# Kernel tuning notes

Measured on AMD Instinct MI355X. Metric: run time of the kernel, lower is better.

Reference implementation:

```python
import jax, jax.numpy as jnp
import numpy as np

DIM = 768   # embedding dim
NH = 12     # num heads
HD = DIM // NH  # head dim = 64
WS = 14     # window size
EPS = 1e-5  # nn.LayerNorm default


def _ln(x, w, b):
    m = jnp.mean(x, -1, keepdims=True)
    v = jnp.var(x, -1, keepdims=True)
    return (x - m) * jax.lax.rsqrt(v + EPS) * w + b


def setup_inputs() -> dict:
    key = jax.random.key(0)
    ks = jax.random.split(key, 8)
    def n(k, shape, s=0.02):
        return jax.random.normal(k, shape, jnp.float32) * s
    return {
        "x": jax.random.normal(ks[0], (4, 64, 64, DIM), jnp.float32),
        "ln1_w": jnp.ones((DIM,), jnp.float32),
        "ln1_b": jnp.zeros((DIM,), jnp.float32),
        "qkv_w": n(ks[1], (DIM, 3 * DIM)),
        "qkv_b": jnp.zeros((3 * DIM,), jnp.float32),
        "proj_w": n(ks[2], (DIM, DIM)),
        "proj_b": jnp.zeros((DIM,), jnp.float32),
        "rel_pos_h": n(ks[3], (2 * WS - 1, HD)),
        "rel_pos_w": n(ks[4], (2 * WS - 1, HD)),
        "ln2_w": jnp.ones((DIM,), jnp.float32),
        "ln2_b": jnp.zeros((DIM,), jnp.float32),
        "fc1_w": n(ks[5], (DIM, 4 * DIM)),
        "fc1_b": jnp.zeros((4 * DIM,), jnp.float32),
        "fc2_w": n(ks[6], (4 * DIM, DIM)),
        "fc2_b": jnp.zeros((DIM,), jnp.float32),
    }


def _block(x, ln1_w, ln1_b, qkv_w, qkv_b, proj_w, proj_b,
           rel_pos_h, rel_pos_w, ln2_w, ln2_b, fc1_w, fc1_b, fc2_w, fc2_b):
    B, H, W, C = x.shape
    shortcut = x
    xn = _ln(x, ln1_w, ln1_b)

    # ---- window partition (pad H,W up to multiples of WS) ----
    pad_h = (-H) % WS
    pad_w = (-W) % WS
    xp = jnp.pad(xn, ((0, 0), (0, pad_h), (0, pad_w), (0, 0)))
    Hp, Wp = H + pad_h, W + pad_w
    nh, nw = Hp // WS, Wp // WS
    xw = xp.reshape(B, nh, WS, nw, WS, C).transpose(0, 1, 3, 2, 4, 5)
    xw = xw.reshape(B * nh * nw, WS, WS, C)  # [Bw, ws, ws, C]
    Bw = B * nh * nw
    N = WS * WS

    # ---- attention with decomposed relative position bias ----
    qkv = xw.reshape(Bw, N, C) @ qkv_w + qkv_b            # [Bw, N, 3C]
    qkv = qkv.reshape(Bw, N, 3, NH, HD).transpose(2, 0, 3, 1, 4)  # [3, Bw, NH, N, HD]
    q, k, v = qkv[0], qkv[1], qkv[2]
    scale = HD ** -0.5
    attn = jnp.einsum("bhnd,bhmd->bhnm", q * scale, k)    # [Bw, NH, N, N]

    # decomposed rel pos: Rh[q_h, k_h, c], Rw[q_w, k_w, c]
    idx = jnp.arange(WS)[:, None] - jnp.arange(WS)[None, :] + (WS - 1)
    Rh = rel_pos_h[idx]  # [ws, ws, HD]
    Rw = rel_pos_w[idx]  # [ws, ws, HD]
    rq = q.reshape(Bw, NH, WS, WS, HD)
    rel_h = jnp.einsum("bnhwc,hkc->bnhwk", rq, Rh)  # over q rows vs k rows
    rel_w = jnp.einsum("bnhwc,wkc->bnhwk", rq, Rw)  # over q cols vs k cols
    attn = (attn.reshape(Bw, NH, WS, WS, WS, WS)
            + rel_h[..., :, None] + rel_w[..., None, :]).reshape(Bw, NH, N, N)

    attn = jax.nn.softmax(attn, axis=-1)
    out = jnp.einsum("bhnm,bhmd->bhnd", attn, v)          # [Bw, NH, N, HD]
    out = out.transpose(0, 2, 1, 3).reshape(Bw, WS, WS, C)
    out = out @ proj_w + proj_b

    # ---- window unpartition + crop padding ----
    out = out.reshape(B, nh, nw, WS, WS, C).transpose(0, 1, 3, 2, 4, 5)
    out = out.reshape(B, Hp, Wp, C)[:, :H, :W, :]

    x = shortcut + out

    # ---- MLP ----
    h = _ln(x, ln2_w, ln2_b)
    h = jax.nn.gelu(h @ fc1_w + fc1_b, approximate=False)
    x = x + (h @ fc2_w + fc2_b)
    return x


def reference(x, ln1_w, ln1_b, qkv_w, qkv_b, proj_w, proj_b,
              rel_pos_h, rel_pos_w, ln2_w, ln2_b, fc1_w, fc1_b, fc2_w, fc2_b):
    return _block(x, ln1_w, ln1_b, qkv_w, qkv_b, proj_w, proj_b,
                  rel_pos_h, rel_pos_w, ln2_w, ln2_b, fc1_w, fc1_b, fc2_w, fc2_b)
```

## Files before the change

kernel.cpp:

```cpp
#include <hip/hip_runtime.h>

typedef unsigned short u16;
typedef __bf16 bf16x8_t __attribute__((ext_vector_type(8)));
typedef float f32x4_t __attribute__((ext_vector_type(4)));

__device__ __forceinline__ float bf2f(u16 u) {
    union { unsigned u; float f; } c; c.u = ((unsigned)u) << 16; return c.f;
}
__device__ __forceinline__ u16 f2bf(float f) {
    union { float f; unsigned u; } c; c.f = f;
    unsigned u = c.u;
    unsigned r = (u + 0x7FFFu + ((u >> 16) & 1u)) >> 16;
    return (u16)r;
}

__device__ __forceinline__ void gld16(const u16* g, u16* l) {
    __builtin_amdgcn_global_load_lds(
        (const __attribute__((address_space(1))) unsigned*)g,
        (__attribute__((address_space(3))) unsigned*)l, 16, 0, 0);
}

__global__ __launch_bounds__(256) void ln1_window(
    const float* __restrict__ x, const float* __restrict__ w, const float* __restrict__ b,
    u16* __restrict__ out, int row0)
{
    int wv = threadIdx.x >> 6, lane = threadIdx.x & 63;
    int lrow = blockIdx.x * 4 + wv;
    int wr = row0 + lrow;
    int wb = wr / 196, t = wr % 196;
    int gh = ((wb % 25) / 5) * 14 + t / 14;
    int gw = (wb % 5) * 14 + t % 14;
    size_t orow = (size_t)lrow * 768;
    if (gh >= 64 || gw >= 64) {
        uint2 zz; zz.x = 0u; zz.y = 0u;
        for (int seg = 0; seg < 3; seg++)
            *(uint2*)&out[orow + seg * 256 + lane * 4] = zz;
        return;
    }
    size_t base = (size_t)(((wb / 25) * 64 + gh) * 64 + gw) * 768;
    f32x4_t v[3];
    float s = 0.f, sq = 0.f;
    for (int seg = 0; seg < 3; seg++) {
        v[seg] = *(const f32x4_t*)&x[base + seg * 256 + lane * 4];
        for (int j = 0; j < 4; j++) { s += v[seg][j]; sq += v[seg][j] * v[seg][j]; }
    }
    for (int o = 32; o > 0; o >>= 1) { s += __shfl_xor(s, o); sq += __shfl_xor(sq, o); }
    float mean = s * (1.0f / 768.0f);
    float var  = sq * (1.0f / 768.0f) - mean * mean;
    float inv  = rsqrtf(var + 1e-5f);
    for (int seg = 0; seg < 3; seg++) {
        f32x4_t w4 = *(const f32x4_t*)&w[seg * 256 + lane * 4];
        f32x4_t b4 = *(const f32x4_t*)&b[seg * 256 + lane * 4];
        u16 o0 = f2bf((v[seg][0] - mean) * inv * w4[0] + b4[0]);
        u16 o1 = f2bf((v[seg][1] - mean) * inv * w4[1] + b4[1]);
        u16 o2 = f2bf((v[seg][2] - mean) * inv * w4[2] + b4[2]);
        u16 o3 = f2bf((v[seg][3] - mean) * inv * w4[3] + b4[3]);
        uint2 pv; pv.x = (unsigned)o0 | ((unsigned)o1 << 16);
        pv.y = (unsigned)o2 | ((unsigned)o3 << 16);
        *(uint2*)&out[orow + seg * 256 + lane * 4] = pv;
    }
}

__global__ __launch_bounds__(256) void ln2_chunk(
    const float* __restrict__ xin, const float* __restrict__ w, const float* __restrict__ b,
    u16* __restrict__ out)
{
    int wv = threadIdx.x >> 6, lane = threadIdx.x & 63;
    int row = blockIdx.x * 4 + wv;
    size_t base = (size_t)row * 768;
    f32x4_t v[3];
    float s = 0.f, sq = 0.f;
    for (int seg = 0; seg < 3; seg++) {
        v[seg] = *(const f32x4_t*)&xin[base + seg * 256 + lane * 4];
        for (int j = 0; j < 4; j++) { s += v[seg][j]; sq += v[seg][j] * v[seg][j]; }
    }
    for (int o = 32; o > 0; o >>= 1) { s += __shfl_xor(s, o); sq += __shfl_xor(sq, o); }
    float mean = s * (1.0f / 768.0f);
    float var  = sq * (1.0f / 768.0f) - mean * mean;
    float inv  = rsqrtf(var + 1e-5f);
    for (int seg = 0; seg < 3; seg++) {
        f32x4_t w4 = *(const f32x4_t*)&w[seg * 256 + lane * 4];
        f32x4_t b4 = *(const f32x4_t*)&b[seg * 256 + lane * 4];
        u16 o0 = f2bf((v[seg][0] - mean) * inv * w4[0] + b4[0]);
        u16 o1 = f2bf((v[seg][1] - mean) * inv * w4[1] + b4[1]);
        u16 o2 = f2bf((v[seg][2] - mean) * inv * w4[2] + b4[2]);
        u16 o3 = f2bf((v[seg][3] - mean) * inv * w4[3] + b4[3]);
        uint2 pv; pv.x = (unsigned)o0 | ((unsigned)o1 << 16);
        pv.y = (unsigned)o2 | ((unsigned)o3 << 16);
        *(uint2*)&out[base + seg * 256 + lane * 4] = pv;
    }
}

__global__ __launch_bounds__(256) void transpose_wf(
    const float* __restrict__ in, u16* __restrict__ out, int K, int N)
{
    __shared__ u16 t[32][33];
    __shared__ u16 tt[32][32];
    int n0 = blockIdx.x * 32, k0 = blockIdx.y * 32;
    int tx = threadIdx.x & 31, ty = threadIdx.x >> 5;
    for (int q = 0; q < 4; q++) {
        int k = k0 + ty + q * 8, n = n0 + tx;
        t[ty + q * 8][tx] = (k < K && n < N) ? f2bf(in[(size_t)k * N + n]) : (u16)0;
    }
    __syncthreads();
    for (int q = 0; q < 4; q++) tt[ty + q * 8][tx] = t[tx][ty + q * 8];
    __syncthreads();
    if (threadIdx.x < 128) {
        int r = threadIdx.x >> 2, c8 = (threadIdx.x & 3) << 3;
        int n = n0 + r, k = k0 + c8;
        if (n < N && k < K)
            *(uint4*)&out[(size_t)n * K + k] = *(const uint4*)&tt[r][c8];
    }
}

__global__ __launch_bounds__(256) void build_relT(
    const float* __restrict__ rh, const float* __restrict__ rw, u16* __restrict__ out)
{
    int i = blockIdx.x * 256 + threadIdx.x;
    int r = i >> 6, c = i & 63;
    float v = (r < 27) ? rh[r * 64 + c] : (r < 54 ? rw[(r - 27) * 64 + c] : 0.f);
    out[i] = f2bf(v);
}

__global__ __launch_bounds__(256) void build_vt(
    const u16* __restrict__ qkvc, u16* __restrict__ vt)
{
    int z = blockIdx.x;
    int wb = z / 12, h = z % 12;
    __shared__ u16 t[64][232];
    int tid = threadIdx.x;
    for (int base = 0; base < 196; base += 4) {
        int m = base + (tid >> 6);
        int d = tid & 63;
        t[d][m] = qkvc[(size_t)(wb * 196 + m) * 2304 + 1536 + h * 64 + d];
    }
    for (int idx = tid; idx < 28 * 64; idx += 256) {
        int m = 196 + idx / 64, d = idx % 64;
        t[d][m] = 0;
    }
    __syncthreads();
    size_t ob = (size_t)z * 64 * 224;
    for (int idx = tid; idx < 64 * 28; idx += 256) {
        int d = idx / 28, c8 = (idx % 28) << 3;
        *(uint4*)&vt[ob + (size_t)d * 224 + c8] = *(const uint4*)&t[d][c8];
    }
}

__global__ __launch_bounds__(256) void softmax_rel2(
    u16* __restrict__ S, const u16* __restrict__ G2)
{
    int z = blockIdx.y;
    int wv = threadIdx.x >> 6, lane = threadIdx.x & 63;
    int nbase = blockIdx.x * 28 + wv * 7;
    for (int i = 0; i < 7; i++) {
        int n = nbase + i;
        size_t srow = (size_t)z * 196 * 224 + (size_t)n * 224;
        const u16* g2 = G2 + (size_t)z * 196 * 64 + (size_t)n * 64;
        int qh = n / 14, qw = n % 14;
        float s[4];
        for (int c = 0; c < 4; c++) {
            int m = c * 64 + lane;
            if (m < 196) {
                int kk = m / 14, jj = m % 14;
                float bh = bf2f(g2[qh - kk + 13]);
                float bw = bf2f(g2[27 + qw - jj + 13]);
                s[c] = 0.125f * bf2f(S[srow + m]) + bh + bw;
            } else s[c] = -1e30f;
        }
        float mx = fmaxf(fmaxf(s[0], s[1]), fmaxf(s[2], s[3]));
        for (int o = 32; o > 0; o >>= 1) mx = fmaxf(mx, __shfl_xor(mx, o));
        float e[4], sm = 0.f;
        for (int c = 0; c < 4; c++) {
            int m = c * 64 + lane;
            e[c] = (m < 196) ? expf(s[c] - mx) : 0.f;
            sm += e[c];
        }
        for (int o = 32; o > 0; o >>= 1) sm += __shfl_xor(sm, o);
        float inv = 1.0f / sm;
        for (int c = 0; c < 4; c++) {
            int m = c * 64 + lane;
            if (m < 224) S[srow + m] = f2bf(e[c] * inv);
        }
    }
}

__device__ __forceinline__ int swz_off(int row, int kcElem) {
    return row * 32 + (kcElem ^ (((row >> 1) & 3) << 3));
}

template <int MODE>
__global__ __launch_bounds__(256, (MODE == 1 || MODE == 2 || MODE == 6) ? 3 : 4)
void gemm_nt(
    const u16* __restrict__ Aall, const u16* __restrict__ Ball,
    const float* __restrict__ bias, const float* xf,
    u16* __restrict__ Cb, float* Cf, int M, int row0)
{
    constexpr int BK = 32;
    constexpr bool DEEP = (MODE == 1 || MODE == 2 || MODE == 6);
    int N, K, lda, ldb;
    size_t aoff = 0, boff = 0, coff = 0;
    if constexpr (MODE == 0) { N = 2304; K = 768; lda = 768; ldb = 768; }
    else if constexpr (MODE == 1) {
        N = 196; K = 64; lda = 2304; ldb = 2304;
        int z = blockIdx.z;
        aoff = (size_t)(z / 12) * 196 * 2304 + (size_t)(z % 12) * 64;
        boff = aoff + 768;
        coff = (size_t)z * 196 * 224;
    } else if constexpr (MODE == 2) {
        N = 64; K = 224; lda = 224; ldb = 224;
        int z = blockIdx.z;
        aoff = (size_t)z * 196 * 224;
        boff = (size_t)z * 64 * 224;
        coff = (size_t)(z / 12) * 196 * 768 + (size_t)(z % 12) * 64;
    } else if constexpr (MODE == 3) { N = 768; K = 768; lda = 768; ldb = 768; }
    else if constexpr (MODE == 4) { N = 3072; K = 768; lda = 768; ldb = 768; }
    else if constexpr (MODE == 6) {
        N = 64; K = 64; lda = 2304; ldb = 64;
        int z = blockIdx.z;
        aoff = (size_t)(z / 12) * 196 * 2304 + (size_t)(z % 12) * 64;
        boff = 0;
        coff = (size_t)z * 196 * 64;
    }
    else { N = 768; K = 3072; lda = 3072; ldb = 3072; }

    constexpr int NBUF = DEEP ? 3 : 2;
    __shared__ __align__(16) u16 smem[NBUF * 8192];

    int tid = threadIdx.x, wid = tid >> 6, lane = tid & 63;
    int quad = lane >> 4, l16 = lane & 15;

    int bx = blockIdx.x, by = blockIdx.y;
    if constexpr (MODE != 1 && MODE != 2 && MODE != 6) {
        int gX = gridDim.x;
        int nwg = gX * gridDim.y;
        int orig = by * gX + bx;
        int q = nwg >> 3, r = nwg & 7;
        int xcd = orig & 7, idx = orig >> 3;
        int wg = (xcd < r ? xcd * (q + 1) : r * (q + 1) + (xcd - r) * q) + idx;
        bx = wg % gX; by = wg / gX;
    }
    int m_tile = by * 128, n_tile = bx * 128;
    int wm0 = (wid >> 1) * 64, wn0 = (wid & 1) * 64;

    const u16* A = Aall + aoff;
    const u16* B = Ball + boff;

    const u16* gA[2]; const u16* gB[2];
    int loff[2];
    {
        int s = lane & 3, rofs = lane >> 2;
        for (int j = 0; j < 2; j++) {
            int r0 = wid * 32 + j * 16;
            int rr = r0 + rofs;
            int xr = (rr >> 1) & 3;
            int colo = ((s ^ xr) << 3);
            int am = m_tile + rr; if (am > M - 1) am = M - 1;
            int bn = n_tile + rr; if (bn > N - 1) bn = N - 1;
            gA[j] = A + (size_t)am * lda + colo;
            gB[j] = B + (size_t)bn * ldb + colo;
            loff[j] = r0 * 32;
        }
    }

    f32x4_t acc[4][4];
    f32x4_t z4 = {0.f, 0.f, 0.f, 0.f};
    for (int mt = 0; mt < 4; mt++)
        for (int nt = 0; nt < 4; nt++) acc[mt][nt] = z4;

    if constexpr (!DEEP) {
        for (int j = 0; j < 2; j++) {
            gld16(gA[j], smem + loff[j]);
            gld16(gB[j], smem + 4096 + loff[j]);
        }
        int cur = 0;
        for (int k0 = 0; k0 < K; k0 += BK) {
            __syncthreads();
            int boffc = cur << 13;
            if (k0 + BK < K) {
                int boffn = boffc ^ 8192;
                for (int j = 0; j < 2; j++) {
                    gld16(gA[j] + k0 + BK, smem + boffn + loff[j]);
                    gld16(gB[j] + k0 + BK, smem + boffn + 4096 + loff[j]);
                }
            }
            const u16* Ac = smem + boffc;
            const u16* Bc = smem + boffc + 4096;
            bf16x8_t af[4], bfv[4];
            for (int t = 0; t < 4; t++) {
                int ar = wm0 + t * 16 + l16;
                int br = wn0 + t * 16 + l16;
                af[t]  = *(const bf16x8_t*)&Ac[swz_off(ar, quad * 8)];
                bfv[t] = *(const bf16x8_t*)&Bc[swz_off(br, quad * 8)];
            }
            for (int mt = 0; mt < 4; mt++)
                for (int nt = 0; nt < 4; nt++)
                    acc[mt][nt] = __builtin_amdgcn_mfma_f32_16x16x32_bf16(
                        af[mt], bfv[nt], acc[mt][nt], 0, 0, 0);
            cur ^= 1;
        }
    } else {
        int nsteps = K / BK;
        for (int j = 0; j < 2; j++) {
            gld16(gA[j], smem + loff[j]);
            gld16(gB[j], smem + 4096 + loff[j]);
        }
        for (int j = 0; j < 2; j++) {
            gld16(gA[j] + BK, smem + 8192 + loff[j]);
            gld16(gB[j] + BK, smem + 12288 + loff[j]);
        }
        int cur = 0;
        for (int k = 0; k < nsteps; k++) {
            if (k + 1 < nsteps) {
                asm volatile("s_waitcnt vmcnt(4)" ::: "memory");
            } else {
                asm volatile("s_waitcnt vmcnt(0)" ::: "memory");
            }
            __builtin_amdgcn_sched_barrier(0);
            __builtin_amdgcn_s_barrier();
            __builtin_amdgcn_sched_barrier(0);
            if (k + 2 < nsteps) {
                int nb = cur + 2; if (nb >= 3) nb -= 3;
                u16* dst = smem + nb * 8192;
                int kn = (k + 2) * BK;
                for (int j = 0; j < 2; j++) {
                    gld16(gA[j] + kn, dst + loff[j]);
                    gld16(gB[j] + kn, dst + 4096 + loff[j]);
                }
            }
            const u16* Ac = smem + cur * 8192;
            const u16* Bc = Ac + 4096;
            bf16x8_t af[4], bfv[4];
            for (int t = 0; t < 4; t++) {
                int ar = wm0 + t * 16 + l16;
                int br = wn0 + t * 16 + l16;
                af[t]  = *(const bf16x8_t*)&Ac[swz_off(ar, quad * 8)];
                bfv[t] = *(const bf16x8_t*)&Bc[swz_off(br, quad * 8)];
            }
            for (int mt = 0; mt < 4; mt++)
                for (int nt = 0; nt < 4; nt++)
                    acc[mt][nt] = __builtin_amdgcn_mfma_f32_16x16x32_bf16(
                        af[mt], bfv[nt], acc[mt][nt], 0, 0, 0);
            cur++; if (cur >= 3) cur -= 3;
        }
    }

    if constexpr (MODE == 0 || MODE == 1 || MODE == 2 || MODE == 4 || MODE == 6) {
        u16* Cs = smem;
        int ldc = (MODE == 0) ? 2304 : (MODE == 1) ? 224 : (MODE == 2) ? 768
                : (MODE == 6) ? 64 : 3072;
        int colmax = (MODE == 1) ? 224 : N;
        for (int half = 0; half < 2; half++) {
            __syncthreads();
            if ((wm0 >> 6) == half) {
                for (int mt = 0; mt < 4; mt++) {
                    int rl = mt * 16 + quad * 4;
                    for (int nt = 0; nt < 4; nt++) {
                        int cl = wn0 + nt * 16 + l16;
                        int col = n_tile + cl;
                        for (int rg = 0; rg < 4; rg++) {
                            float v = acc[mt][nt][rg];
                            u16 o;
                            if constexpr (MODE == 0) o = f2bf(v + bias[col]);
                            else if constexpr (MODE == 4) {
                                float g = v + bias[col];
                                o = f2bf(0.5f * g * (1.0f + erff(g * 0.70710678118f)));
                            } else o = f2bf(v);
                            Cs[(rl + rg) * 136 + cl] = o;
                        }
                    }
                }
            }
            __syncthreads();
            for (int it = 0; it < 4; it++) {
                int chunk = tid + it * 256;
                int r = chunk >> 4, c8 = (chunk & 15) << 3;
                int grow = m_tile + half * 64 + r, gcol = n_tile + c8;
                if (grow >= M || gcol >= colmax) continue;
                *(uint4*)&Cb[coff + (size_t)grow * ldc + gcol] =
                    *(const uint4*)&Cs[r * 136 + c8];
            }
        }
    } else {
        float* Cfs = (float*)smem;
        for (int q = 0; q < 4; q++) {
            __syncthreads();
            if ((wm0 >> 6) == (q >> 1)) {
                for (int mt2 = 0; mt2 < 2; mt2++) {
                    int mt = (q & 1) * 2 + mt2;
                    int rloc = mt2 * 16 + quad * 4;
                    for (int nt = 0; nt < 4; nt++) {
                        int cl = wn0 + nt * 16 + l16;
                        for (int rg = 0; rg < 4; rg++)
                            Cfs[(rloc + rg) * 132 + cl] = acc[mt][nt][rg];
                    }
                }
            }
            __syncthreads();
            for (int it = 0; it < 4; it++) {
                int chunk = tid + it * 256;
                int r = chunk >> 5, c4 = (chunk & 31) << 2;
                int grow = m_tile + q * 32 + r;
                int gcol = n_tile + c4;
                if (grow >= M || gcol >= N) continue;
                f32x4_t v4 = *(const f32x4_t*)&Cfs[r * 132 + c4];
                f32x4_t b4 = *(const f32x4_t*)&bias[gcol];
                if constexpr (MODE == 5) {
                    size_t idx = (size_t)(row0 + grow) * 768 + gcol;
                    f32x4_t x4 = *(const f32x4_t*)&xf[idx];
                    f32x4_t o4;
                    for (int j = 0; j < 4; j++) o4[j] = v4[j] + x4[j] + b4[j];
                    *(f32x4_t*)&Cf[idx] = o4;
                } else {
                    int wr = row0 + grow;
                    int wb2 = wr / 196, t2 = wr % 196;
                    int gh = ((wb2 % 25) / 5) * 14 + t2 / 14;
                    int gw = (wb2 % 5) * 14 + t2 % 14;
                    if (gh < 64 && gw < 64) {
                        size_t g = (size_t)(((wb2 / 25) * 64 + gh) * 64 + gw) * 768 + gcol;
                        f32x4_t x4 = *(const f32x4_t*)&xf[g];
                        f32x4_t o4;
                        for (int j = 0; j < 4; j++) o4[j] = v4[j] + x4[j] + b4[j];
                        *(f32x4_t*)&Cf[g] = o4;
                    }
                }
            }
        }
    }
}

extern "C" void kernel_launch(void* const* d_in, const int* in_sizes, int n_in,
                              void* d_out, int out_size, void* d_ws, size_t ws_size,
                              hipStream_t stream)
{
    (void)in_sizes; (void)n_in; (void)out_size;
    const float* x      = (const float*)d_in[0];
    const float* ln1_w  = (const float*)d_in[1];
    const float* ln1_b  = (const float*)d_in[2];
    const float* qkv_w  = (const float*)d_in[3];
    const float* qkv_b  = (const float*)d_in[4];
    const float* proj_w = (const float*)d_in[5];
    const float* proj_b = (const float*)d_in[6];
    const float* rel_h  = (const float*)d_in[7];
    const float* rel_w  = (const float*)d_in[8];
    const float* ln2_w  = (const float*)d_in[9];
    const float* ln2_b  = (const float*)d_in[10];
    const float* fc1_w  = (const float*)d_in[11];
    const float* fc1_b  = (const float*)d_in[12];
    const float* fc2_w  = (const float*)d_in[13];
    const float* fc2_b  = (const float*)d_in[14];

    const size_t WT = 14155776ull + 8192ull;
    char* ws = (char*)d_ws;
    u16* qkvT  = (u16*)ws;
    u16* projT = qkvT + 2304 * 768;
    u16* fc1T  = projT + 768 * 768;
    u16* fc2T  = fc1T + 3072 * 768;
    u16* relT  = fc2T + 3072 * 768;
    char* scratch = ws + WT;
    size_t avail = (ws_size > WT) ? (ws_size - WT) : 0;

    const size_t perW = 3204096ull;
    static const int wc_cand[8] = {100, 50, 25, 20, 10, 5, 2, 1};
    int Wc = 1;
    for (int i = 0; i < 8; i++) {
        if ((size_t)wc_cand[i] * perW <= avail) { Wc = wc_cand[i]; break; }
    }
    static const int rm_cand[8] = {16384, 8192, 4096, 2048, 1024, 512, 256, 128};
    int Rm = 128;
    for (int i = 0; i < 8; i++) {
        if ((size_t)rm_cand[i] * 7680ull <= avail) { Rm = rm_cand[i]; break; }
    }

    u16* lnwc  = (u16*)scratch;
    u16* qkvc  = (u16*)(scratch + (size_t)Wc * 301056ull);
    u16* Sc    = (u16*)(scratch + (size_t)Wc * 1204224ull);
    u16* vtc   = (u16*)(scratch + (size_t)Wc * 2257920ull);
    u16* attnc = (u16*)(scratch + (size_t)Wc * 2601984ull);
    u16* G2c   = (u16*)(scratch + (size_t)Wc * 2903040ull);
    u16* hbuf  = (u16*)scratch;
    u16* xn2c  = (u16*)(scratch + (size_t)Rm * 6144ull);
    float* dout = (float*)d_out;

    transpose_wf<<<dim3(72, 24), 256, 0, stream>>>(qkv_w, qkvT, 768, 2304);
    transpose_wf<<<dim3(24, 24), 256, 0, stream>>>(proj_w, projT, 768, 768);
    transpose_wf<<<dim3(96, 24), 256, 0, stream>>>(fc1_w, fc1T, 768, 3072);
    transpose_wf<<<dim3(24, 96), 256, 0, stream>>>(fc2_w, fc2T, 3072, 768);
    build_relT<<<16, 256, 0, stream>>>(rel_h, rel_w, relT);

    int nch = 100 / Wc;
    int rows = Wc * 196;
    int gy = (rows + 127) / 128;
    for (int c = 0; c < nch; c++) {
        int r0 = c * rows;
        ln1_window<<<rows / 4, 256, 0, stream>>>(x, ln1_w, ln1_b, lnwc, r0);
        gemm_nt<0><<<dim3(18, gy), 256, 0, stream>>>(
            lnwc, qkvT, qkv_b, nullptr, qkvc, nullptr, rows, 0);
        gemm_nt<1><<<dim3(2, 2, Wc * 12), 256, 0, stream>>>(
            qkvc, qkvc, nullptr, nullptr, Sc, nullptr, 196, 0);
        gemm_nt<6><<<dim3(1, 2, Wc * 12), 256, 0, stream>>>(
            qkvc, relT, nullptr, nullptr, G2c, nullptr, 196, 0);
        build_vt<<<Wc * 12, 256, 0, stream>>>(qkvc, vtc);
        softmax_rel2<<<dim3(7, Wc * 12), 256, 0, stream>>>(Sc, G2c);
        gemm_nt<2><<<dim3(1, 2, Wc * 12), 256, 0, stream>>>(
            Sc, vtc, nullptr, nullptr, attnc, nullptr, 196, 0);
        gemm_nt<3><<<dim3(6, gy), 256, 0, stream>>>(
            attnc, projT, proj_b, x, nullptr, dout, rows, r0);
    }

    int nm = 16384 / Rm;
    for (int c = 0; c < nm; c++) {
        int r0 = c * Rm;
        ln2_chunk<<<Rm / 4, 256, 0, stream>>>(dout + (size_t)r0 * 768, ln2_w, ln2_b, xn2c);
        gemm_nt<4><<<dim3(24, Rm / 128), 256, 0, stream>>>(
            xn2c, fc1T, fc1_b, nullptr, hbuf, nullptr, Rm, 0);
        gemm_nt<5><<<dim3(6, Rm / 128), 256, 0, stream>>>(
            hbuf, fc2T, fc2_b, dout, nullptr, dout, Rm, r0);
    }
}
```

Before: 715.0 us.

## Fuse rel-pos projection GEMM into QK^T GEMM and reuse qkv buffer for attention output

The q·relT product is now computed inside the QK^T GEMM by appending the 54 rel-pos rows as extra B columns (N grows from 196 to 250, S row stride to 256), removing the separate MODE 6 launch and the G2 buffer. Softmax reads the bias terms from the extra columns of the same S row. The attention output is written back into the qkv buffer's q slot (stride 2304), so the projection GEMM reads it from there and the attn buffer goes away, which shrinks per-window scratch and may allow larger chunks. The cost is wider S rows and more columns per QK^T tile.

Result: slower. 753.6 us (+5.4%).

```diff
diff --git a/kernel.cpp b/kernel.cpp
--- a/kernel.cpp
+++ b/kernel.cpp
@@ -147,23 +147,22 @@
 }
 
 __global__ __launch_bounds__(256) void softmax_rel2(
-    u16* __restrict__ S, const u16* __restrict__ G2)
+    u16* __restrict__ S)
 {
     int z = blockIdx.y;
     int wv = threadIdx.x >> 6, lane = threadIdx.x & 63;
     int nbase = blockIdx.x * 28 + wv * 7;
     for (int i = 0; i < 7; i++) {
         int n = nbase + i;
-        size_t srow = (size_t)z * 196 * 224 + (size_t)n * 224;
-        const u16* g2 = G2 + (size_t)z * 196 * 64 + (size_t)n * 64;
+        size_t srow = (size_t)z * 196 * 256 + (size_t)n * 256;
         int qh = n / 14, qw = n % 14;
         float s[4];
         for (int c = 0; c < 4; c++) {
             int m = c * 64 + lane;
             if (m < 196) {
                 int kk = m / 14, jj = m % 14;
-                float bh = bf2f(g2[qh - kk + 13]);
-                float bw = bf2f(g2[27 + qw - jj + 13]);
+                float bh = bf2f(S[srow + 209 + qh - kk]);
+                float bw = bf2f(S[srow + 236 + qw - jj]);
                 s[c] = 0.125f * bf2f(S[srow + m]) + bh + bw;
             } else s[c] = -1e30f;
         }
@@ -189,38 +188,31 @@
 }
 
 template <int MODE>
-__global__ __launch_bounds__(256, (MODE == 1 || MODE == 2 || MODE == 6) ? 3 : 4)
+__global__ __launch_bounds__(256, (MODE == 1 || MODE == 2) ? 3 : 4)
 void gemm_nt(
     const u16* __restrict__ Aall, const u16* __restrict__ Ball,
     const float* __restrict__ bias, const float* xf,
     u16* __restrict__ Cb, float* Cf, int M, int row0)
 {
     constexpr int BK = 32;
-    constexpr bool DEEP = (MODE == 1 || MODE == 2 || MODE == 6);
+    constexpr bool DEEP = (MODE == 1 || MODE == 2);
     int N, K, lda, ldb;
     size_t aoff = 0, boff = 0, coff = 0;
     if constexpr (MODE == 0) { N = 2304; K = 768; lda = 768; ldb = 768; }
     else if constexpr (MODE == 1) {
-        N = 196; K = 64; lda = 2304; ldb = 2304;
+        N = 250; K = 64; lda = 2304; ldb = 2304;
         int z = blockIdx.z;
         aoff = (size_t)(z / 12) * 196 * 2304 + (size_t)(z % 12) * 64;
         boff = aoff + 768;
-        coff = (size_t)z * 196 * 224;
+        coff = (size_t)z * 196 * 256;
     } else if constexpr (MODE == 2) {
-        N = 64; K = 224; lda = 224; ldb = 224;
+        N = 64; K = 224; lda = 256; ldb = 224;
         int z = blockIdx.z;
-        aoff = (size_t)z * 196 * 224;
+        aoff = (size_t)z * 196 * 256;
         boff = (size_t)z * 64 * 224;
-        coff = (size_t)(z / 12) * 196 * 768 + (size_t)(z % 12) * 64;
-    } else if constexpr (MODE == 3) { N = 768; K = 768; lda = 768; ldb = 768; }
+        coff = (size_t)(z / 12) * 196 * 2304 + (size_t)(z % 12) * 64;
+    } else if constexpr (MODE == 3) { N = 768; K = 768; lda = 2304; ldb = 768; }
     else if constexpr (MODE == 4) { N = 3072; K = 768; lda = 768; ldb = 768; }
-    else if constexpr (MODE == 6) {
-        N = 64; K = 64; lda = 2304; ldb = 64;
-        int z = blockIdx.z;
-        aoff = (size_t)(z / 12) * 196 * 2304 + (size_t)(z % 12) * 64;
-        boff = 0;
-        coff = (size_t)z * 196 * 64;
-    }
     else { N = 768; K = 3072; lda = 3072; ldb = 3072; }
 
     constexpr int NBUF = DEEP ? 3 : 2;
@@ -230,7 +222,7 @@
     int quad = lane >> 4, l16 = lane & 15;
 
     int bx = blockIdx.x, by = blockIdx.y;
-    if constexpr (MODE != 1 && MODE != 2 && MODE != 6) {
+    if constexpr (MODE != 1 && MODE != 2) {
         int gX = gridDim.x;
         int nwg = gX * gridDim.y;
         int orig = by * gX + bx;
@@ -244,6 +236,8 @@
 
     const u16* A = Aall + aoff;
     const u16* B = Ball + boff;
+    const u16* rT = nullptr;
+    if constexpr (MODE == 1) rT = (const u16*)xf;
 
     const u16* gA[2]; const u16* gB[2];
     int loff[2];
@@ -257,7 +251,11 @@
             int am = m_tile + rr; if (am > M - 1) am = M - 1;
             int bn = n_tile + rr; if (bn > N - 1) bn = N - 1;
             gA[j] = A + (size_t)am * lda + colo;
-            gB[j] = B + (size_t)bn * ldb + colo;
+            if constexpr (MODE == 1)
+                gB[j] = (bn < 196) ? (B + (size_t)bn * 2304 + colo)
+                                   : (rT + (size_t)(bn - 196) * 64 + colo);
+            else
+                gB[j] = B + (size_t)bn * ldb + colo;
             loff[j] = r0 * 32;
         }
     }
@@ -344,11 +342,10 @@
         }
     }
 
-    if constexpr (MODE == 0 || MODE == 1 || MODE == 2 || MODE == 4 || MODE == 6) {
+    if constexpr (MODE == 0 || MODE == 1 || MODE == 2 || MODE == 4) {
         u16* Cs = smem;
-        int ldc = (MODE == 0) ? 2304 : (MODE == 1) ? 224 : (MODE == 2) ? 768
-                : (MODE == 6) ? 64 : 3072;
-        int colmax = (MODE == 1) ? 224 : N;
+        int ldc = (MODE == 0) ? 2304 : (MODE == 1) ? 256 : (MODE == 2) ? 2304 : 3072;
+        int colmax = (MODE == 1) ? 256 : N;
         for (int half = 0; half < 2; half++) {
             __syncthreads();
             if ((wm0 >> 6) == half) {
@@ -459,7 +456,7 @@
     char* scratch = ws + WT;
     size_t avail = (ws_size > WT) ? (ws_size - WT) : 0;
 
-    const size_t perW = 3204096ull;
+    const size_t perW = 2752512ull;
     static const int wc_cand[8] = {100, 50, 25, 20, 10, 5, 2, 1};
     int Wc = 1;
     for (int i = 0; i < 8; i++) {
@@ -474,9 +471,7 @@
     u16* lnwc  = (u16*)scratch;
     u16* qkvc  = (u16*)(scratch + (size_t)Wc * 301056ull);
     u16* Sc    = (u16*)(scratch + (size_t)Wc * 1204224ull);
-    u16* vtc   = (u16*)(scratch + (size_t)Wc * 2257920ull);
-    u16* attnc = (u16*)(scratch + (size_t)Wc * 2601984ull);
-    u16* G2c   = (u16*)(scratch + (size_t)Wc * 2903040ull);
+    u16* vtc   = (u16*)(scratch + (size_t)Wc * 2408448ull);
     u16* hbuf  = (u16*)scratch;
     u16* xn2c  = (u16*)(scratch + (size_t)Rm * 6144ull);
     float* dout = (float*)d_out;
@@ -496,15 +491,13 @@
         gemm_nt<0><<<dim3(18, gy), 256, 0, stream>>>(
             lnwc, qkvT, qkv_b, nullptr, qkvc, nullptr, rows, 0);
         gemm_nt<1><<<dim3(2, 2, Wc * 12), 256, 0, stream>>>(
-            qkvc, qkvc, nullptr, nullptr, Sc, nullptr, 196, 0);
-        gemm_nt<6><<<dim3(1, 2, Wc * 12), 256, 0, stream>>>(
-            qkvc, relT, nullptr, nullptr, G2c, nullptr, 196, 0);
+            qkvc, qkvc, nullptr, (const float*)relT, Sc, nullptr, 196, 0);
         build_vt<<<Wc * 12, 256, 0, stream>>>(qkvc, vtc);
-        softmax_rel2<<<dim3(7, Wc * 12), 256, 0, stream>>>(Sc, G2c);
+        softmax_rel2<<<dim3(7, Wc * 12), 256, 0, stream>>>(Sc);
         gemm_nt<2><<<dim3(1, 2, Wc * 12), 256, 0, stream>>>(
-            Sc, vtc, nullptr, nullptr, attnc, nullptr, 196, 0);
+            Sc, vtc, nullptr, nullptr, qkvc, nullptr, 196, 0);
         gemm_nt<3><<<dim3(6, gy), 256, 0, stream>>>(
-            attnc, projT, proj_b, x, nullptr, dout, rows, r0);
+            qkvc, projT, proj_b, x, nullptr, dout, rows, r0);
     }
 
     int nm = 16384 / Rm;
```
